# Optimization experiments

Measured on AMD Instinct MI355X. Metric: run time of the kernel, lower is better.

The kernel has to match this reference:

```python
import jax, jax.numpy as jnp
import numpy as np

NUM_EMBEDDINGS = 512
EMBEDDING_DIM = 64


def setup_inputs() -> dict:
    key = jax.random.key(0)
    k_in, k_emb = jax.random.split(key)
    inputs = jax.random.normal(k_in, (8, 64, 16, 32, 32), dtype=jnp.float32)
    # matches torch uniform_(-1/K, 1/K) init
    lim = 1.0 / NUM_EMBEDDINGS
    embedding = jax.random.uniform(
        k_emb, (NUM_EMBEDDINGS, EMBEDDING_DIM), dtype=jnp.float32,
        minval=-lim, maxval=lim)
    return {"inputs": inputs, "embedding": embedding}


def reference(inputs, embedding):
    # inputs: (B, C=D, T, H, W); embedding: (K, D)
    x = jnp.transpose(inputs, (0, 2, 3, 4, 1))  # (B, T, H, W, D)
    in_shape = x.shape
    flat = x.reshape(-1, EMBEDDING_DIM)  # (N, D)
    distances = (
        jnp.sum(flat * flat, axis=1, keepdims=True)
        + jnp.sum(embedding * embedding, axis=1)
        - 2.0 * jnp.matmul(flat, embedding.T)
    )  # (N, K)
    # NOTE: original applies softmax to raw (positive) distances, faithfully kept
    weights = jax.nn.softmax(distances, axis=1)
    out = jnp.matmul(weights, embedding).reshape(in_shape)  # (B,T,H,W,D)
    return jnp.transpose(out, (0, 4, 1, 2, 3))  # (B, D, T, H, W)
```

## Files before the change

### kernel.cpp

```cpp
#include <hip/hip_runtime.h>
#include <hip/hip_bf16.h>

typedef __attribute__((ext_vector_type(8))) short short8;
typedef __attribute__((ext_vector_type(4))) short short4v;
typedef __attribute__((ext_vector_type(4))) _Float16 half4;
typedef __attribute__((ext_vector_type(4))) float f32x4;

#define SPW 16384
#define XST 72
#define RW  67
#define LOG2E 1.4426950408889634f

__device__ __forceinline__ float exp2_hw(float f) {
  return __builtin_amdgcn_exp2f(f);
}

__device__ __forceinline__ short bf16s(float f) {
  union { __hip_bfloat16 h; short s; } u;
  u.h = __float2bfloat16(f);
  return u.s;
}

__global__ void prep_all(const float* __restrict__ emb, short8* __restrict__ a1,
                         half4* __restrict__ eb, float* __restrict__ norms) {
  const int f = blockIdx.x * 256 + threadIdx.x;
  if (f < 4096) {
    const int l = f & 63;
    const int s = (f >> 6) & 1;
    const int m = f >> 7;
    const int row = m * 16 + (l & 15);
    const int col0 = s * 32 + (l >> 4) * 8;
    short8 v;
    #pragma unroll
    for (int i = 0; i < 8; ++i)
      v[i] = bf16s(-2.0f * LOG2E * emb[row * 64 + col0 + i]);
    a1[f] = v;
  } else if (f < 12288) {
    const int e = f - 4096;
    const int l = e & 63;
    const int m2 = (e >> 6) & 3;
    const int kt = e >> 8;
    const int d = m2 * 16 + (l & 15);
    const int k0 = kt * 16 + 4 * (l >> 4);
    half4 v;
    #pragma unroll
    for (int i = 0; i < 4; ++i) v[i] = (_Float16)emb[(k0 + i) * 64 + d];
    eb[e] = v;
  } else if (f < 12800) {
    const int k = f - 12288;
    float acc = 0.f;
    #pragma unroll
    for (int d = 0; d < 64; ++d) { float e = emb[k * 64 + d]; acc += e * e; }
    norms[k] = acc * LOG2E;
  }
}

__global__ __launch_bounds__(256, 3) void vq_main(
    const float* __restrict__ x, const short8* __restrict__ a1,
    const half4* __restrict__ eb, const float* __restrict__ norms,
    float* __restrict__ out) {
  __shared__ __align__(16) char lds_raw[35840];
  short* Xl   = reinterpret_cast<short*>(lds_raw);
  float* Rf   = reinterpret_cast<float*>(lds_raw);
  float* denl = reinterpret_cast<float*>(lds_raw + 34304);
  float* rden = reinterpret_cast<float*>(lds_raw + 35328);

  const int t = threadIdx.x;
  const int lane = t & 63;
  const int w = t >> 6;
  const int cg = w & 1;
  const int kg = w >> 1;
  const int l15 = lane & 15;
  const int g = lane >> 4;

  const int tile = blockIdx.x * 128;
  const int b = tile >> 14;
  const int off = tile & 16383;
  const float* xb = x + (size_t)b * (64 * SPW) + off;
  float* ob = out + (size_t)b * (64 * SPW) + off;

  {
    const int n0 = 4 * (t & 15);
    const int d0 = 4 * (t >> 4);
    #pragma unroll
    for (int h = 0; h < 2; ++h) {
      const int nb = h * 64 + n0;
      const float4 r0 = *reinterpret_cast<const float4*>(xb + (size_t)(d0 + 0) * SPW + nb);
      const float4 r1 = *reinterpret_cast<const float4*>(xb + (size_t)(d0 + 1) * SPW + nb);
      const float4 r2 = *reinterpret_cast<const float4*>(xb + (size_t)(d0 + 2) * SPW + nb);
      const float4 r3 = *reinterpret_cast<const float4*>(xb + (size_t)(d0 + 3) * SPW + nb);
      const short4v c0 = {bf16s(r0.x), bf16s(r1.x), bf16s(r2.x), bf16s(r3.x)};
      const short4v c1 = {bf16s(r0.y), bf16s(r1.y), bf16s(r2.y), bf16s(r3.y)};
      const short4v c2 = {bf16s(r0.z), bf16s(r1.z), bf16s(r2.z), bf16s(r3.z)};
      const short4v c3 = {bf16s(r0.w), bf16s(r1.w), bf16s(r2.w), bf16s(r3.w)};
      *reinterpret_cast<short4v*>(&Xl[(nb + 0) * XST + d0]) = c0;
      *reinterpret_cast<short4v*>(&Xl[(nb + 1) * XST + d0]) = c1;
      *reinterpret_cast<short4v*>(&Xl[(nb + 2) * XST + d0]) = c2;
      *reinterpret_cast<short4v*>(&Xl[(nb + 3) * XST + d0]) = c3;
    }
  }
  __syncthreads();

  short8 bx[4][2];
  #pragma unroll
  for (int j = 0; j < 4; ++j) {
    const int base = (cg * 64 + j * 16 + l15) * XST + g * 8;
    bx[j][0] = *reinterpret_cast<const short8*>(&Xl[base]);
    bx[j][1] = *reinterpret_cast<const short8*>(&Xl[base + 32]);
  }

  f32x4 pacc[4][4];
  #pragma unroll
  for (int j = 0; j < 4; ++j)
    #pragma unroll
    for (int m2 = 0; m2 < 4; ++m2) pacc[j][m2] = f32x4{0.f, 0.f, 0.f, 0.f};
  float denp[4] = {0.f, 0.f, 0.f, 0.f};

  const int kbase = kg * 16;
  #pragma unroll
  for (int q = 0; q < 16; ++q) {
    const int kt = kbase + q;
    const short8 a1f0 = a1[(kt * 2 + 0) * 64 + lane];
    const short8 a1f1 = a1[(kt * 2 + 1) * 64 + lane];
    const half4 e0 = eb[(kt * 4 + 0) * 64 + lane];
    const half4 e1 = eb[(kt * 4 + 1) * 64 + lane];
    const half4 e2 = eb[(kt * 4 + 2) * 64 + lane];
    const half4 e3 = eb[(kt * 4 + 3) * 64 + lane];
    const float4 nv = *reinterpret_cast<const float4*>(&norms[kt * 16 + g * 4]);
    #pragma unroll
    for (int j = 0; j < 4; ++j) {
      f32x4 z = {0.f, 0.f, 0.f, 0.f};
      z = __builtin_amdgcn_mfma_f32_16x16x32_bf16(a1f0, bx[j][0], z, 0, 0, 0);
      z = __builtin_amdgcn_mfma_f32_16x16x32_bf16(a1f1, bx[j][1], z, 0, 0, 0);
      const float p0 = exp2_hw(nv.x + z[0]);
      const float p1 = exp2_hw(nv.y + z[1]);
      const float p2 = exp2_hw(nv.z + z[2]);
      const float p3 = exp2_hw(nv.w + z[3]);
      denp[j] += (p0 + p1) + (p2 + p3);
      const half4 pa = {(_Float16)p0, (_Float16)p1, (_Float16)p2, (_Float16)p3};
      pacc[j][0] = __builtin_amdgcn_mfma_f32_16x16x16f16(pa, e0, pacc[j][0], 0, 0, 0);
      pacc[j][1] = __builtin_amdgcn_mfma_f32_16x16x16f16(pa, e1, pacc[j][1], 0, 0, 0);
      pacc[j][2] = __builtin_amdgcn_mfma_f32_16x16x16f16(pa, e2, pacc[j][2], 0, 0, 0);
      pacc[j][3] = __builtin_amdgcn_mfma_f32_16x16x16f16(pa, e3, pacc[j][3], 0, 0, 0);
    }
  }

  #pragma unroll
  for (int j = 0; j < 4; ++j) {
    denp[j] += __shfl_xor(denp[j], 16, 64);
    denp[j] += __shfl_xor(denp[j], 32, 64);
  }
  if (lane < 16) {
    #pragma unroll
    for (int j = 0; j < 4; ++j)
      denl[kg * 128 + cg * 64 + j * 16 + l15] = denp[j];
  }

  if (kg == 0) {
    #pragma unroll
    for (int j = 0; j < 4; ++j)
      #pragma unroll
      for (int m2 = 0; m2 < 4; ++m2)
        #pragma unroll
        for (int r = 0; r < 4; ++r)
          Rf[(cg * 64 + j * 16 + 4 * g + r) * RW + m2 * 16 + l15] = pacc[j][m2][r];
  }
  __syncthreads();

  if (kg == 1) {
    #pragma unroll
    for (int j = 0; j < 4; ++j)
      #pragma unroll
      for (int m2 = 0; m2 < 4; ++m2)
        #pragma unroll
        for (int r = 0; r < 4; ++r)
          Rf[(cg * 64 + j * 16 + 4 * g + r) * RW + m2 * 16 + l15] += pacc[j][m2][r];
  } else {
    rden[t & 127] = 1.0f / (denl[t & 127] + denl[128 + (t & 127)]);
  }
  __syncthreads();

  const int nq = t & 31;
  const int n = 4 * nq;
  const int dh = t >> 5;
  #pragma unroll
  for (int it = 0; it < 8; ++it) {
    const int d = it * 8 + dh;
    const float4 o = {Rf[(n + 0) * RW + d] * rden[n + 0],
                      Rf[(n + 1) * RW + d] * rden[n + 1],
                      Rf[(n + 2) * RW + d] * rden[n + 2],
                      Rf[(n + 3) * RW + d] * rden[n + 3]};
    *reinterpret_cast<float4*>(&ob[(size_t)d * SPW + n]) = o;
  }
}

extern "C" void kernel_launch(void* const* d_in, const int* in_sizes, int n_in,
                              void* d_out, int out_size, void* d_ws, size_t ws_size,
                              hipStream_t stream) {
  (void)in_sizes; (void)n_in; (void)out_size; (void)ws_size;
  const float* x   = (const float*)d_in[0];
  const float* emb = (const float*)d_in[1];
  float* out = (float*)d_out;

  char* ws = (char*)d_ws;
  short8* a1   = (short8*)ws;
  half4*  eb   = (half4*)(ws + 65536);
  float*  norms = (float*)(ws + 131072);

  prep_all<<<50, 256, 0, stream>>>(emb, a1, eb, norms);
  vq_main<<<1024, 256, 0, stream>>>(x, a1, eb, norms, out);
}
```

Before: 40.68 us.

## Use 16x16x32 f16 MFMA for softmax-weighted sum, pairing codebook tiles

The second GEMM (weights times embedding) now uses the K=32 f16 MFMA instead of the K=16 one. Each iteration processes two 16-code tiles, and the prep kernel packs the embedding into matching half8 fragments. Norms are folded into the MFMA accumulator init, and p values are packed with cvt_pkrtz. The aim is to halve the second-GEMM MFMA count and cut per-element add and convert overhead, at the cost of more live registers per iteration and an extra barrier after the LDS fragment loads.

```diff
diff --git a/kernel.cpp b/kernel.cpp
--- a/kernel.cpp
+++ b/kernel.cpp
@@ -3,7 +3,8 @@
 
 typedef __attribute__((ext_vector_type(8))) short short8;
 typedef __attribute__((ext_vector_type(4))) short short4v;
-typedef __attribute__((ext_vector_type(4))) _Float16 half4;
+typedef __attribute__((ext_vector_type(8))) _Float16 half8;
+typedef __attribute__((ext_vector_type(2))) __fp16 fp16x2;
 typedef __attribute__((ext_vector_type(4))) float f32x4;
 
 #define SPW 16384
@@ -21,33 +22,36 @@
   return u.s;
 }
 
-__global__ void prep_all(const float* __restrict__ emb, short8* __restrict__ a1,
-                         half4* __restrict__ eb, float* __restrict__ norms) {
+__global__ void prep_all(const float* __restrict__ emb, short8* __restrict__ a1b,
+                         half8* __restrict__ eb3, float* __restrict__ norms) {
   const int f = blockIdx.x * 256 + threadIdx.x;
   if (f < 4096) {
-    const int l = f & 63;
-    const int s = (f >> 6) & 1;
-    const int m = f >> 7;
-    const int row = m * 16 + (l & 15);
-    const int col0 = s * 32 + (l >> 4) * 8;
+    const int s = f & 1;
+    const int lane = (f >> 1) & 63;
+    const int kt = f >> 7;
+    const int row = kt * 16 + (lane & 15);
+    const int col0 = s * 32 + (lane >> 4) * 8;
     short8 v;
     #pragma unroll
     for (int i = 0; i < 8; ++i)
       v[i] = bf16s(-2.0f * LOG2E * emb[row * 64 + col0 + i]);
-    a1[f] = v;
-  } else if (f < 12288) {
+    a1b[f] = v;
+  } else if (f < 8192) {
     const int e = f - 4096;
-    const int l = e & 63;
-    const int m2 = (e >> 6) & 3;
-    const int kt = e >> 8;
-    const int d = m2 * 16 + (l & 15);
-    const int k0 = kt * 16 + 4 * (l >> 4);
-    half4 v;
-    #pragma unroll
-    for (int i = 0; i < 4; ++i) v[i] = (_Float16)emb[(k0 + i) * 64 + d];
-    eb[e] = v;
-  } else if (f < 12800) {
-    const int k = f - 12288;
+    const int m2 = e & 3;
+    const int lane = (e >> 2) & 63;
+    const int pr = e >> 8;
+    const int g = lane >> 4;
+    const int d = m2 * 16 + (lane & 15);
+    half8 v;
+    #pragma unroll
+    for (int i = 0; i < 8; ++i) {
+      const int k = (i < 4) ? (pr * 32 + 4 * g + i) : (pr * 32 + 16 + 4 * g + (i - 4));
+      v[i] = (_Float16)emb[k * 64 + d];
+    }
+    eb3[e] = v;
+  } else if (f < 8704) {
+    const int k = f - 8192;
     float acc = 0.f;
     #pragma unroll
     for (int d = 0; d < 64; ++d) { float e = emb[k * 64 + d]; acc += e * e; }
@@ -56,8 +60,8 @@
 }
 
 __global__ __launch_bounds__(256, 3) void vq_main(
-    const float* __restrict__ x, const short8* __restrict__ a1,
-    const half4* __restrict__ eb, const float* __restrict__ norms,
+    const float* __restrict__ x, const short8* __restrict__ a1b,
+    const half8* __restrict__ eb3, const float* __restrict__ norms,
     float* __restrict__ out) {
   __shared__ __align__(16) char lds_raw[35840];
   short* Xl   = reinterpret_cast<short*>(lds_raw);
@@ -108,6 +112,7 @@
     bx[j][0] = *reinterpret_cast<const short8*>(&Xl[base]);
     bx[j][1] = *reinterpret_cast<const short8*>(&Xl[base + 32]);
   }
+  __syncthreads();
 
   f32x4 pacc[4][4];
   #pragma unroll
@@ -116,32 +121,50 @@
     for (int m2 = 0; m2 < 4; ++m2) pacc[j][m2] = f32x4{0.f, 0.f, 0.f, 0.f};
   float denp[4] = {0.f, 0.f, 0.f, 0.f};
 
-  const int kbase = kg * 16;
-  #pragma unroll
-  for (int q = 0; q < 16; ++q) {
-    const int kt = kbase + q;
-    const short8 a1f0 = a1[(kt * 2 + 0) * 64 + lane];
-    const short8 a1f1 = a1[(kt * 2 + 1) * 64 + lane];
-    const half4 e0 = eb[(kt * 4 + 0) * 64 + lane];
-    const half4 e1 = eb[(kt * 4 + 1) * 64 + lane];
-    const half4 e2 = eb[(kt * 4 + 2) * 64 + lane];
-    const half4 e3 = eb[(kt * 4 + 3) * 64 + lane];
-    const float4 nv = *reinterpret_cast<const float4*>(&norms[kt * 16 + g * 4]);
+  #pragma unroll
+  for (int p = 0; p < 8; ++p) {
+    const int pr = kg * 8 + p;
+    const int ktA = pr * 2;
+    const short8* ap = &a1b[(ktA * 64 + lane) * 2];
+    const short8 aA0 = ap[0];
+    const short8 aA1 = ap[1];
+    const short8 aB0 = ap[128];
+    const short8 aB1 = ap[129];
+    const half8* ep = &eb3[(pr * 64 + lane) * 4];
+    const half8 e0 = ep[0];
+    const half8 e1 = ep[1];
+    const half8 e2 = ep[2];
+    const half8 e3 = ep[3];
+    const float4 nvA = *reinterpret_cast<const float4*>(&norms[ktA * 16 + g * 4]);
+    const float4 nvB = *reinterpret_cast<const float4*>(&norms[ktA * 16 + 16 + g * 4]);
+
     #pragma unroll
     for (int j = 0; j < 4; ++j) {
-      f32x4 z = {0.f, 0.f, 0.f, 0.f};
-      z = __builtin_amdgcn_mfma_f32_16x16x32_bf16(a1f0, bx[j][0], z, 0, 0, 0);
-      z = __builtin_amdgcn_mfma_f32_16x16x32_bf16(a1f1, bx[j][1], z, 0, 0, 0);
-      const float p0 = exp2_hw(nv.x + z[0]);
-      const float p1 = exp2_hw(nv.y + z[1]);
-      const float p2 = exp2_hw(nv.z + z[2]);
-      const float p3 = exp2_hw(nv.w + z[3]);
-      denp[j] += (p0 + p1) + (p2 + p3);
-      const half4 pa = {(_Float16)p0, (_Float16)p1, (_Float16)p2, (_Float16)p3};
-      pacc[j][0] = __builtin_amdgcn_mfma_f32_16x16x16f16(pa, e0, pacc[j][0], 0, 0, 0);
-      pacc[j][1] = __builtin_amdgcn_mfma_f32_16x16x16f16(pa, e1, pacc[j][1], 0, 0, 0);
-      pacc[j][2] = __builtin_amdgcn_mfma_f32_16x16x16f16(pa, e2, pacc[j][2], 0, 0, 0);
-      pacc[j][3] = __builtin_amdgcn_mfma_f32_16x16x16f16(pa, e3, pacc[j][3], 0, 0, 0);
+      f32x4 zA = {nvA.x, nvA.y, nvA.z, nvA.w};
+      zA = __builtin_amdgcn_mfma_f32_16x16x32_bf16(aA0, bx[j][0], zA, 0, 0, 0);
+      zA = __builtin_amdgcn_mfma_f32_16x16x32_bf16(aA1, bx[j][1], zA, 0, 0, 0);
+      f32x4 zB = {nvB.x, nvB.y, nvB.z, nvB.w};
+      zB = __builtin_amdgcn_mfma_f32_16x16x32_bf16(aB0, bx[j][0], zB, 0, 0, 0);
+      zB = __builtin_amdgcn_mfma_f32_16x16x32_bf16(aB1, bx[j][1], zB, 0, 0, 0);
+      const float p0 = exp2_hw(zA[0]);
+      const float p1 = exp2_hw(zA[1]);
+      const float p2 = exp2_hw(zA[2]);
+      const float p3 = exp2_hw(zA[3]);
+      const float p4 = exp2_hw(zB[0]);
+      const float p5 = exp2_hw(zB[1]);
+      const float p6 = exp2_hw(zB[2]);
+      const float p7 = exp2_hw(zB[3]);
+      denp[j] += ((p0 + p1) + (p2 + p3)) + ((p4 + p5) + (p6 + p7));
+      union { fp16x2 h2[4]; half8 h8; } pk;
+      pk.h2[0] = __builtin_amdgcn_cvt_pkrtz(p0, p1);
+      pk.h2[1] = __builtin_amdgcn_cvt_pkrtz(p2, p3);
+      pk.h2[2] = __builtin_amdgcn_cvt_pkrtz(p4, p5);
+      pk.h2[3] = __builtin_amdgcn_cvt_pkrtz(p6, p7);
+      const half8 pa = pk.h8;
+      pacc[j][0] = __builtin_amdgcn_mfma_f32_16x16x32_f16(pa, e0, pacc[j][0], 0, 0, 0);
+      pacc[j][1] = __builtin_amdgcn_mfma_f32_16x16x32_f16(pa, e1, pacc[j][1], 0, 0, 0);
+      pacc[j][2] = __builtin_amdgcn_mfma_f32_16x16x32_f16(pa, e2, pacc[j][2], 0, 0, 0);
+      pacc[j][3] = __builtin_amdgcn_mfma_f32_16x16x32_f16(pa, e3, pacc[j][3], 0, 0, 0);
     }
   }
 
@@ -203,10 +226,10 @@
   float* out = (float*)d_out;
 
   char* ws = (char*)d_ws;
-  short8* a1   = (short8*)ws;
-  half4*  eb   = (half4*)(ws + 65536);
+  short8* a1b  = (short8*)ws;
+  half8*  eb3  = (half8*)(ws + 65536);
   float*  norms = (float*)(ws + 131072);
 
-  prep_all<<<50, 256, 0, stream>>>(emb, a1, eb, norms);
-  vq_main<<<1024, 256, 0, stream>>>(x, a1, eb, norms, out);
-}
+  prep_all<<<34, 256, 0, stream>>>(emb, a1b, eb3, norms);
+  vq_main<<<1024, 256, 0, stream>>>(x, a1b, eb3, norms, out);
+}
```

Result: slower. 46.63 us (+14.6%).
